# Optimization experiments

Hardware: AMD Instinct MI355X
Metric: run time of the kernel (lower is better)

## Reference

```python
import jax, jax.numpy as jnp
import numpy as np

B, SC, ST = 16, 512, 512
DP, DC = 256, 128
D = DP + 2 * DC          # 512 = d_model
H, L, DFF = 8, 2, 2048
NCAT, NCONT = 1000, 2048


def sin_embed(vals, d, scale=1000.0):
    # vectorized sinusoidal_time_embedding: even dims -> sin(angle), odd dims -> cos(angle)
    i = jnp.arange(d, dtype=jnp.float32)
    ang = vals.astype(jnp.float32)[..., None] / jnp.power(scale, i / d)
    return jnp.where(i % 2 == 0, jnp.sin(ang), jnp.cos(ang))


def layer_norm(x, g, b, eps=1e-5):
    m = jnp.mean(x, -1, keepdims=True)
    v = jnp.mean(jnp.square(x - m), -1, keepdims=True)
    return (x - m) / jnp.sqrt(v + eps) * g + b


def setup_inputs() -> dict:
    key = jax.random.key(0)
    ks = jax.random.split(key, 16)
    s = 0.02
    def n(k, shape, scale=s):
        return jax.random.normal(k, shape, dtype=jnp.float32) * scale
    return {
        "context_cat": jax.random.randint(ks[0], (B, SC), 0, NCAT),
        "context_time": jax.random.uniform(ks[1], (B, SC), dtype=jnp.float32) * 100.0,
        "context_f0": jax.random.uniform(ks[2], (B, SC), dtype=jnp.float32) * 500.0,
        "target_cat": jax.random.randint(ks[3], (B, ST), 0, NCAT),
        "target_time": jax.random.uniform(ks[4], (B, ST), dtype=jnp.float32) * 100.0,
        "target_f0": jax.random.uniform(ks[5], (B, ST), dtype=jnp.float32) * 500.0,
        "cat_table": n(ks[6], (NCAT, DP), 1.0),
        "cont_table": sin_embed(jnp.arange(NCONT, dtype=jnp.float32), DC),  # frozen sin table
        "pad_emb": n(ks[7], (D,), 1.0),
        "Wq": n(ks[8], (L, D, D)), "bq": jnp.zeros((L, D)),
        "Wk": n(ks[9], (L, D, D)), "bk": jnp.zeros((L, D)),
        "Wv": n(ks[10], (L, D, D)), "bv": jnp.zeros((L, D)),
        "Wo": n(ks[11], (L, D, D)), "bo": jnp.zeros((L, D)),
        "ln1g": jnp.ones((L, D)), "ln1b": jnp.zeros((L, D)),
        "ln2g": jnp.ones((L, D)), "ln2b": jnp.zeros((L, D)),
        "W1": n(ks[12], (L, D, DFF)), "b1": jnp.zeros((L, DFF)),
        "W2": n(ks[13], (L, DFF, D)), "b2": jnp.zeros((L, D)),
    }


def reference(context_cat, context_time, context_f0, target_cat, target_time, target_f0,
              cat_table, cont_table, pad_emb,
              Wq, bq, Wk, bk, Wv, bv, Wo, bo,
              ln1g, ln1b, ln2g, ln2b, W1, b1, W2, b2):
    def embed(cat, tm, f0):
        pad = cat < 0
        e = jnp.concatenate(
            [cat_table[jnp.maximum(cat, 0)], sin_embed(tm, DC), sin_embed(f0, DC)], axis=-1)
        return jnp.where(pad[..., None], pad_emb, e), pad

    ce, cp = embed(context_cat, context_time, context_f0)
    te, tp = embed(target_cat, target_time, target_f0)
    x = jnp.concatenate([ce, te], axis=1)                       # [B, SC+ST, D]
    bias = jnp.where(jnp.concatenate([cp, tp], 1), -1e9, 0.0)[:, None, None, :]
    hd = D // H
    inv_sqrt = 1.0 / np.sqrt(hd).astype(np.float32)

    def step(h, p):
        wq, bq_, wk, bk_, wv, bv_, wo, bo_, g1, c1, g2, c2, w1, d1, w2, d2 = p
        Bn, S, _ = h.shape
        q = (h @ wq + bq_).reshape(Bn, S, H, hd)
        k = (h @ wk + bk_).reshape(Bn, S, H, hd)
        v = (h @ wv + bv_).reshape(Bn, S, H, hd)
        scores = jnp.einsum('bqhd,bkhd->bhqk', q, k) * inv_sqrt + bias
        attn = jax.nn.softmax(scores, axis=-1)
        o = jnp.einsum('bhqk,bkhd->bqhd', attn, v).reshape(Bn, S, D)
        h = layer_norm(h + o @ wo + bo_, g1, c1)                # post-norm (torch default)
        f = jax.nn.relu(h @ w1 + d1) @ w2 + d2
        return layer_norm(h + f, g2, c2), None

    x, _ = jax.lax.scan(step, x, (Wq, bq, Wk, bk, Wv, bv, Wo, bo,
                                  ln1g, ln1b, ln2g, ln2b, W1, b1, W2, b2))
    out = x[:, SC:, :]
    pred_cat = out[..., :DP] @ cat_table.T
    pred_time = out[..., DP:DP + DC] @ cont_table.T
    pred_f0 = out[..., DP + DC:] @ cont_table.T
    return pred_cat, pred_time, pred_f0
```

## Files before the change

### kernel.cpp

```cpp
#include <hip/hip_runtime.h>


typedef _Float16 half8 __attribute__((ext_vector_type(8)));
typedef _Float16 half4 __attribute__((ext_vector_type(4)));
typedef float f32x4 __attribute__((ext_vector_type(4)));
typedef unsigned int uint2v __attribute__((ext_vector_type(2)));
typedef unsigned int uint4v __attribute__((ext_vector_type(4)));

__device__ __forceinline__ void gl2lds16(const _Float16* g, _Float16* l) {
    __builtin_amdgcn_global_load_lds(
        (const __attribute__((address_space(1))) void*)g,
        (__attribute__((address_space(3))) void*)l, 16, 0, 0);
}

__global__ void cast_f32_f16_k(const float* __restrict__ in, _Float16* __restrict__ out,
                               long nsrc, long ntot) {
    long i = (long)blockIdx.x * blockDim.x + threadIdx.x;
    long stride = (long)gridDim.x * blockDim.x;
    for (; i < ntot; i += stride) out[i] = i < nsrc ? (_Float16)in[i] : (_Float16)0.f;
}

__global__ void tcast_k(const float* __restrict__ in, _Float16* __restrict__ out,
                        int R, int C, long zs, int rowoff) {
    __shared__ float tile[32][33];
    long z = blockIdx.z;
    const float* src = in + z * (long)R * C;
    _Float16* dst = out + z * zs + (long)rowoff * R;
    int c0 = blockIdx.x * 32, r0 = blockIdx.y * 32;
    for (int i = threadIdx.y; i < 32; i += 8)
        tile[i][threadIdx.x] = src[(long)(r0 + i) * C + c0 + threadIdx.x];
    __syncthreads();
    for (int i = threadIdx.y; i < 32; i += 8)
        dst[(long)(c0 + i) * R + r0 + threadIdx.x] = (_Float16)tile[threadIdx.x][i];
}

__global__ void bcat_k(const float* __restrict__ bq, const float* __restrict__ bk,
                       const float* __restrict__ bv, float* __restrict__ out, int L) {
    int i = blockIdx.x * 256 + threadIdx.x;
    if (i >= L * 1536) return;
    int l = i / 1536, j = i - l * 1536;
    float v = j < 512 ? bq[l * 512 + j] : (j < 1024 ? bk[l * 512 + j - 512] : bv[l * 512 + j - 1024]);
    out[i] = v;
}

__global__ void vtrans_k(const _Float16* __restrict__ qkv, _Float16* __restrict__ vT) {
    __shared__ _Float16 tile[32][33];
    int bh = blockIdx.z; int b = bh >> 3, h = bh & 7;
    int s0 = blockIdx.x * 32, d0 = blockIdx.y * 32;
    const _Float16* src = qkv + ((long)b * 1024) * 1536 + 1024 + h * 64;
    _Float16* dst = vT + (long)bh * 64 * 1024;
    for (int i = threadIdx.y; i < 32; i += 8)
        tile[i][threadIdx.x] = src[(long)(s0 + i) * 1536 + d0 + threadIdx.x];
    __syncthreads();
    for (int i = threadIdx.y; i < 32; i += 8)
        dst[(long)(d0 + i) * 1024 + s0 + threadIdx.x] = tile[threadIdx.x][i];
}

__global__ __launch_bounds__(128) void embed_k(
    const int* __restrict__ ccat, const float* __restrict__ ctime, const float* __restrict__ cf0,
    const int* __restrict__ tcat, const float* __restrict__ ttime, const float* __restrict__ tf0,
    const float* __restrict__ cat_table, const float* __restrict__ pad_emb,
    _Float16* __restrict__ xb, float* __restrict__ biasKey) {
    int t = blockIdx.x;
    int b = t >> 10, s = t & 1023;
    int j = b * 512 + (s & 511);
    int cat; float tm, f0;
    if (s < 512) { cat = ccat[j]; tm = ctime[j]; f0 = cf0[j]; }
    else         { cat = tcat[j]; tm = ttime[j]; f0 = tf0[j]; }
    bool pad = cat < 0;
    if (threadIdx.x == 0) biasKey[t] = pad ? -1e9f : 0.f;
    int c = cat < 0 ? 0 : cat;
    half4 h4;
    #pragma unroll
    for (int u = 0; u < 4; u++) {
        int d = threadIdx.x * 4 + u;
        float val;
        if (pad) val = pad_emb[d];
        else if (d < 256) val = cat_table[(long)c * 256 + d];
        else {
            float base = (d < 384) ? tm : f0;
            int i = (d < 384) ? (d - 256) : (d - 384);
            float ang = base / powf(1000.f, (float)i * (1.f / 128.f));
            val = (i & 1) ? cosf(ang) : sinf(ang);
        }
        h4[u] = (_Float16)val;
    }
    *(half4*)&xb[(long)t * 512 + threadIdx.x * 4] = h4;
}

__global__ __launch_bounds__(256) void layernorm_k(
    const _Float16* __restrict__ in, _Float16* __restrict__ out,
    const float* __restrict__ g, const float* __restrict__ beta) {
    long row = blockIdx.x;
    int tid = threadIdx.x;
    const unsigned* rw = (const unsigned*)(in + row * 512);
    unsigned wo = rw[tid];
    float v0 = (float)(_Float16)__builtin_bit_cast(_Float16, (unsigned short)(wo & 0xffff));
    float v1 = (float)(_Float16)__builtin_bit_cast(_Float16, (unsigned short)(wo >> 16));
    float s = v0 + v1, q = v0 * v0 + v1 * v1;
    #pragma unroll
    for (int o = 32; o; o >>= 1) { s += __shfl_down(s, o); q += __shfl_down(q, o); }
    __shared__ float rs[4], rq[4];
    if ((tid & 63) == 0) { rs[tid >> 6] = s; rq[tid >> 6] = q; }
    __syncthreads();
    s = rs[0] + rs[1] + rs[2] + rs[3];
    q = rq[0] + rq[1] + rq[2] + rq[3];
    float mean = s * (1.f / 512.f);
    float var = q * (1.f / 512.f) - mean * mean;
    float rstd = rsqrtf(var + 1e-5f);
    float y0 = (v0 - mean) * rstd * g[tid * 2] + beta[tid * 2];
    float y1 = (v1 - mean) * rstd * g[tid * 2 + 1] + beta[tid * 2 + 1];
    unsigned short u0 = __builtin_bit_cast(unsigned short, (_Float16)y0);
    unsigned short u1 = __builtin_bit_cast(unsigned short, (_Float16)y1);
    ((unsigned*)(out + row * 512))[tid] = (unsigned)u0 | ((unsigned)u1 << 16);
}

__global__ __launch_bounds__(512, 4) void flash_k(
    const _Float16* __restrict__ QKV, const _Float16* __restrict__ VT,
    const float* __restrict__ biasKey, _Float16* __restrict__ O) {
    const int S = 1024, D = 512, LDQ = 1536, NT = 16;
    int bh = blockIdx.x; int b = bh >> 3, h = bh & 7;
    int qt = blockIdx.y;
    int tid = threadIdx.x, w = tid >> 6, lane = tid & 63;
    int g = lane >> 4, q15 = lane & 15;

    __shared__ __align__(16) _Float16 Ks[2][64 * 64];
    __shared__ __align__(16) _Float16 VTs[2][64 * 64];
    __shared__ __align__(16) float biasLds[1024];

    {
        const float* bsrc = biasKey + (long)b * S;
        biasLds[tid]       = bsrc[tid] * 1.442695041f;
        biasLds[tid + 512] = bsrc[tid + 512] * 1.442695041f;
    }

    int qrow = qt * 128 + w * 16 + q15;
    const _Float16* qp = QKV + ((long)(b * S + qrow)) * LDQ + h * 64 + g * 8;
    half8 qf[2];
    qf[0] = *(const half8*)(qp);
    qf[1] = *(const half8*)(qp + 32);
    const _Float16 qsc = (_Float16)0.1803368801f;
    #pragma unroll
    for (int kk = 0; kk < 2; kk++)
        #pragma unroll
        for (int i = 0; i < 8; i++) qf[kk][i] *= qsc;

    const _Float16* kbase = QKV + 512 + ((long)b * S) * LDQ + h * 64;
    const _Float16* vbase = VT + (long)bh * 64 * S;

    auto stageK = [&](int buf, int kt) {
        int row = tid >> 3, p = tid & 7;
        int s = p ^ (row & 7);
        gl2lds16(kbase + (long)(kt * 64 + row) * LDQ + s * 8, &Ks[buf][tid * 8]);
    };
    auto stageV = [&](int buf, int kt) {
        int row = tid >> 3, p = tid & 7;
        int s = p ^ (row & 7);
        gl2lds16(vbase + (long)row * S + kt * 64 + s * 8, &VTs[buf][tid * 8]);
    };

    f32x4 acc_o[4];
    #pragma unroll
    for (int i = 0; i < 4; i++)
        #pragma unroll
        for (int r = 0; r < 4; r++) acc_o[i][r] = 0.f;
    float m_run = -1e30f, l_run = 0.f;
    bool gOdd = (g & 1) != 0;

    auto QK = [&](int kt, f32x4 (&s)[4]) {
        #pragma unroll
        for (int mf = 0; mf < 4; mf++)
            s[mf] = *(const f32x4*)&biasLds[kt * 64 + mf * 16 + g * 4];
        int buf = kt & 1;
        __builtin_amdgcn_s_setprio(1);
        #pragma unroll
        for (int kk = 0; kk < 2; kk++)
            #pragma unroll
            for (int mf = 0; mf < 4; mf++) {
                int row = mf * 16 + q15;
                half8 kf = *(const half8*)&Ks[buf][row * 64 + (((kk * 4 + g) ^ (row & 7)) * 8)];
                s[mf] = __builtin_amdgcn_mfma_f32_16x16x32_f16(kf, qf[kk], s[mf], 0, 0, 0);
            }
        __builtin_amdgcn_s_setprio(0);
    };

    auto SMPV = [&](int kt, f32x4 (&s)[4]) {
        float t0 = fmaxf(fmaxf(s[0][0], s[0][1]), fmaxf(s[0][2], s[0][3]));
        float t1 = fmaxf(fmaxf(s[1][0], s[1][1]), fmaxf(s[1][2], s[1][3]));
        float t2 = fmaxf(fmaxf(s[2][0], s[2][1]), fmaxf(s[2][2], s[2][3]));
        float t3 = fmaxf(fmaxf(s[3][0], s[3][1]), fmaxf(s[3][2], s[3][3]));
        float mt = fmaxf(fmaxf(t0, t1), fmaxf(t2, t3));
        mt = fmaxf(mt, __shfl_xor(mt, 16));
        mt = fmaxf(mt, __shfl_xor(mt, 32));

        float rsum = 0.f;
        if (__all(mt - m_run <= 8.f)) {
            #pragma unroll
            for (int mf = 0; mf < 4; mf++)
                #pragma unroll
                for (int r = 0; r < 4; r++) {
                    float p = exp2f(s[mf][r] - m_run);
                    s[mf][r] = p; rsum += p;
                }
        } else {
            float m_new = fmaxf(m_run, mt);
            float scale = exp2f(m_run - m_new);
            #pragma unroll
            for (int mf = 0; mf < 4; mf++)
                #pragma unroll
                for (int r = 0; r < 4; r++) {
                    float p = exp2f(s[mf][r] - m_new);
                    s[mf][r] = p; rsum += p;
                }
            float sc[4];
            #pragma unroll
            for (int r = 0; r < 4; r++) sc[r] = __shfl(scale, g * 4 + r);
            #pragma unroll
            for (int nf = 0; nf < 4; nf++)
                #pragma unroll
                for (int r = 0; r < 4; r++) acc_o[nf][r] *= sc[r];
            l_run *= scale;
            m_run = m_new;
        }
        rsum += __shfl_xor(rsum, 16);
        rsum += __shfl_xor(rsum, 32);
        l_run += rsum;

        unsigned pk[4][2];
        #pragma unroll
        for (int mf = 0; mf < 4; mf++) {
            auto h0 = __builtin_amdgcn_cvt_pkrtz(s[mf][0], s[mf][1]);
            auto h1 = __builtin_amdgcn_cvt_pkrtz(s[mf][2], s[mf][3]);
            pk[mf][0] = __builtin_bit_cast(unsigned, h0);
            pk[mf][1] = __builtin_bit_cast(unsigned, h1);
        }

        int buf = kt & 1;
        #pragma unroll
        for (int kk = 0; kk < 2; kk++) {
            unsigned wA[2], wB[2];
            #pragma unroll
            for (int wi = 0; wi < 2; wi++) {
                uint2v r2 = __builtin_amdgcn_permlane32_swap(
                    pk[2 * kk][wi], pk[2 * kk + 1][wi], false, false);
                unsigned na = r2[0];
                unsigned nb = r2[1];
                unsigned sa = (unsigned)__builtin_amdgcn_ds_swizzle((int)na, 0x401F);
                unsigned sb = (unsigned)__builtin_amdgcn_ds_swizzle((int)nb, 0x401F);
                wA[wi] = gOdd ? sb : na;
                wB[wi] = gOdd ? nb : sa;
            }
            uint4v paw;
            paw[0] = wA[0]; paw[1] = wA[1]; paw[2] = wB[0]; paw[3] = wB[1];
            half8 pa = __builtin_bit_cast(half8, paw);
            __builtin_amdgcn_s_setprio(1);
            #pragma unroll
            for (int nf = 0; nf < 4; nf++) {
                int row = nf * 16 + q15;
                half8 vf = *(const half8*)&VTs[buf][row * 64 + (((kk * 4 + g) ^ (row & 7)) * 8)];
                acc_o[nf] = __builtin_amdgcn_mfma_f32_16x16x32_f16(pa, vf, acc_o[nf], 0, 0, 0);
            }
            __builtin_amdgcn_s_setprio(0);
        }
    };

    f32x4 sA[4], sB[4];
    stageK(0, 0); stageV(0, 0); stageK(1, 1);
    __syncthreads();
    QK(0, sA);

    for (int t = 0; t < NT; t += 2) {
        __syncthreads();
        if (t + 2 < NT) stageK(t & 1, t + 2);
        if (t + 1 < NT) stageV((t + 1) & 1, t + 1);
        if (t + 1 < NT) QK(t + 1, sB);
        SMPV(t, sA);
        __syncthreads();
        if (t + 3 < NT) stageK((t + 1) & 1, t + 3);
        if (t + 2 < NT) stageV(t & 1, t + 2);
        if (t + 2 < NT) QK(t + 2, sA);
        SMPV(t + 1, sB);
    }

    float linv = 1.f / l_run;
    float lv[4];
    #pragma unroll
    for (int r = 0; r < 4; r++) lv[r] = __shfl(linv, g * 4 + r);
    _Float16* obase = O + ((long)(b * S + qt * 128 + w * 16)) * D + h * 64;
    #pragma unroll
    for (int nf = 0; nf < 4; nf++)
        #pragma unroll
        for (int r = 0; r < 4; r++) {
            int row = g * 4 + r;
            obase[(long)row * D + nf * 16 + q15] = (_Float16)(acc_o[nf][r] * lv[r]);
        }
}

template<int NBUF>
__global__ __launch_bounds__(256) void gemm_nt(
    const _Float16* __restrict__ A, long lda, long sA1, long sA2,
    const _Float16* __restrict__ Bm, long ldb, long sB1, long sB2,
    float* Cf, _Float16* Cb, long ldc, long sC1, long sC2,
    const float* __restrict__ bias, long sb1, long sb2,
    const _Float16* resid,
    int M, int N, int K, int Z2, float alpha, int relu) {
    int z = blockIdx.z;
    int z1 = z / Z2, z2 = z - z1 * Z2;
    A  += z1 * sA1 + z2 * sA2;
    Bm += z1 * sB1 + z2 * sB2;
    long coff = z1 * sC1 + z2 * sC2;
    if (bias) bias += z1 * sb1 + z2 * sb2;

    int gx = gridDim.x;
    int nwg = gx * gridDim.y;
    int bid = blockIdx.y * gx + blockIdx.x;
    int q = nwg >> 3, r = nwg & 7;
    int xcd = bid & 7, ii = bid >> 3;
    int swz = (xcd < r ? xcd * (q + 1) : r * (q + 1) + (xcd - r) * q) + ii;
    int m0 = (swz / gx) * 128;
    int n0 = (swz % gx) * 128;

    __shared__ __align__(16) _Float16 As[NBUF][128 * 32];
    __shared__ __align__(16) _Float16 Bs[NBUF][128 * 32];

    int tid = threadIdx.x;
    int lane = tid & 63;
    int w = tid >> 6;
    int wr = (w >> 1) << 6;
    int wc = (w & 1) << 6;

    f32x4 acc[4][4];
    #pragma unroll
    for (int i = 0; i < 4; i++)
        #pragma unroll
        for (int jj = 0; jj < 4; jj++) { acc[i][jj][0] = 0.f; acc[i][jj][1] = 0.f; acc[i][jj][2] = 0.f; acc[i][jj][3] = 0.f; }

    int fr = lane & 15;
    int g = lane >> 4;
    int rs8 = (g ^ (fr & 3)) * 8;

    auto stage = [&](int buf, int kt) {
        #pragma unroll
        for (int i = 0; i < 2; i++) {
            int idx = tid + i * 256;
            int row = idx >> 2, s = idx & 3;
            int sg = s ^ (row & 3);
            gl2lds16(A + (long)(m0 + row) * lda + kt * 32 + sg * 8, &As[buf][idx * 8]);
            gl2lds16(Bm + (long)(n0 + row) * ldb + kt * 32 + sg * 8, &Bs[buf][idx * 8]);
        }
    };

    auto compute = [&](int cur) {
        half8 af[4], bfv[4];
        #pragma unroll
        for (int m = 0; m < 4; m++) af[m] = *(const half8*)&As[cur][(wr + m * 16 + fr) * 32 + rs8];
        #pragma unroll
        for (int n = 0; n < 4; n++) bfv[n] = *(const half8*)&Bs[cur][(wc + n * 16 + fr) * 32 + rs8];
        #pragma unroll
        for (int m = 0; m < 4; m++)
            #pragma unroll
            for (int n = 0; n < 4; n++)
                acc[m][n] = __builtin_amdgcn_mfma_f32_16x16x32_f16(af[m], bfv[n], acc[m][n], 0, 0, 0);
    };

    int nk = K >> 5;
    if constexpr (NBUF == 2) {
        stage(0, 0);
        for (int t = 0; t < nk; ++t) {
            __builtin_amdgcn_s_barrier();
            if (t + 1 < nk) {
                stage((t + 1) & 1, t + 1);
                asm volatile("s_waitcnt vmcnt(4)" ::: "memory");
            } else {
                asm volatile("s_waitcnt vmcnt(0)" ::: "memory");
            }
            __builtin_amdgcn_s_barrier();
            __builtin_amdgcn_sched_barrier(0);
            compute(t & 1);
        }
    } else {
        stage(0, 0);
        if (nk > 1) stage(1, 1);
        if (nk > 2) stage(2, 2);
        for (int t = 0; t < nk; ++t) {
            if (t + 2 < nk)      asm volatile("s_waitcnt vmcnt(8)" ::: "memory");
            else if (t + 1 < nk) asm volatile("s_waitcnt vmcnt(4)" ::: "memory");
            else                 asm volatile("s_waitcnt vmcnt(0)" ::: "memory");
            __builtin_amdgcn_s_barrier();
            __builtin_amdgcn_sched_barrier(0);
            if (t + 3 < nk) stage((t + 3) & 3, t + 3);
            compute(t & 3);
        }
    }

    int fq = lane >> 4;
    #pragma unroll
    for (int m = 0; m < 4; m++) {
        #pragma unroll
        for (int jj = 0; jj < 4; jj++) {
            long row = m0 + wr + m * 16 + fq * 4 + jj;
            #pragma unroll
            for (int n = 0; n < 4; n++) {
                int col = n0 + wc + n * 16 + fr;
                if (col < N) {
                    float v = acc[m][n][jj] * alpha;
                    if (bias) v += bias[col];
                    long o = coff + row * ldc + col;
                    if (resid) v += (float)resid[o];
                    if (relu) v = fmaxf(v, 0.f);
                    if (Cf) Cf[o] = v;
                    if (Cb) Cb[o] = (_Float16)v;
                }
            }
        }
    }
}

extern "C" void kernel_launch(void* const* d_in, const int* in_sizes, int n_in,
                              void* d_out, int out_size, void* d_ws, size_t ws_size,
                              hipStream_t stream) {
    const int Bn = 16, S = 1024, D = 512, H = 8, L = 2, DFF = 2048, NCAT = 1000, NCONT = 2048;
    const long M = (long)Bn * S;

    const int*   ccat      = (const int*)d_in[0];
    const float* ctime     = (const float*)d_in[1];
    const float* cf0       = (const float*)d_in[2];
    const int*   tcat      = (const int*)d_in[3];
    const float* ttime     = (const float*)d_in[4];
    const float* tf0       = (const float*)d_in[5];
    const float* cat_table = (const float*)d_in[6];
    const float* cont_tab  = (const float*)d_in[7];
    const float* pad_emb   = (const float*)d_in[8];
    const float* Wq = (const float*)d_in[9];
    const float* bq = (const float*)d_in[10];
    const float* Wk = (const float*)d_in[11];
    const float* bk = (const float*)d_in[12];
    const float* Wv = (const float*)d_in[13];
    const float* bv = (const float*)d_in[14];
    const float* Wo = (const float*)d_in[15];
    const float* bo = (const float*)d_in[16];
    const float* ln1g = (const float*)d_in[17];
    const float* ln1b = (const float*)d_in[18];
    const float* ln2g = (const float*)d_in[19];
    const float* ln2b = (const float*)d_in[20];
    const float* W1 = (const float*)d_in[21];
    const float* b1 = (const float*)d_in[22];
    const float* W2 = (const float*)d_in[23];
    const float* b2 = (const float*)d_in[24];

    char* wsb = (char*)d_ws;
    size_t off = 0;
    auto alloc = [&](size_t bytes) -> void* {
        off = (off + 255) & ~(size_t)255;
        void* p = wsb + off; off += bytes; return p;
    };

    _Float16*  xb      = (_Float16*)alloc(M * D * 2);
    _Float16*  tb      = (_Float16*)alloc(M * D * 2);
    _Float16*  hb      = (_Float16*)alloc(M * D * 2);
    _Float16*  qkv     = (_Float16*)alloc(M * 3 * D * 2);
    _Float16*  vT      = (_Float16*)alloc(M * D * 2);
    _Float16*  ob      = (_Float16*)alloc(M * D * 2);
    float*     biasKey = (float*)alloc(M * 4);
    _Float16*  WqkvT = (_Float16*)alloc((size_t)L * 3 * D * D * 2);
    float*     bqkv  = (float*)alloc((size_t)L * 3 * D * 4);
    _Float16*  WoT  = (_Float16*)alloc((size_t)L * D * D * 2);
    _Float16*  W1T  = (_Float16*)alloc((size_t)L * D * DFF * 2);
    _Float16*  W2T  = (_Float16*)alloc((size_t)L * DFF * D * 2);
    _Float16*  catT = (_Float16*)alloc((size_t)1024 * 256 * 2);
    _Float16*  conT = (_Float16*)alloc((size_t)NCONT * 128 * 2);

    size_t need_ffh = (size_t)M * DFF * 2;
    _Float16* ffh;
    size_t offAl = (off + 255) & ~(size_t)255;
    if (offAl + need_ffh <= ws_size) ffh = (_Float16*)alloc(need_ffh);
    else ffh = (_Float16*)d_out;

    auto gemm = [&](const _Float16* A, long lda, long sA1, long sA2,
                    const _Float16* Bm, long ldb, long sB1, long sB2,
                    float* Cf, _Float16* Cb, long ldc, long sC1, long sC2,
                    const float* bias, long sb1, long sb2,
                    const _Float16* resid, int Mm, int Nn, int Kk,
                    int Z1, int Z2, float alpha, int relu, int deep) {
        dim3 gdim((Nn + 127) / 128, (Mm + 127) / 128, Z1 * Z2);
        if (deep)
            gemm_nt<4><<<gdim, 256, 0, stream>>>(A, lda, sA1, sA2, Bm, ldb, sB1, sB2,
                                                 Cf, Cb, ldc, sC1, sC2, bias, sb1, sb2,
                                                 resid, Mm, Nn, Kk, Z2, alpha, relu);
        else
            gemm_nt<2><<<gdim, 256, 0, stream>>>(A, lda, sA1, sA2, Bm, ldb, sB1, sB2,
                                                 Cf, Cb, ldc, sC1, sC2, bias, sb1, sb2,
                                                 resid, Mm, Nn, Kk, Z2, alpha, relu);
    };

    dim3 tb8(32, 8);
    tcast_k<<<dim3(D / 32, D / 32, L), tb8, 0, stream>>>(Wq, WqkvT, D, D, (long)3 * D * D, 0);
    tcast_k<<<dim3(D / 32, D / 32, L), tb8, 0, stream>>>(Wk, WqkvT, D, D, (long)3 * D * D, D);
    tcast_k<<<dim3(D / 32, D / 32, L), tb8, 0, stream>>>(Wv, WqkvT, D, D, (long)3 * D * D, 2 * D);
    bcat_k<<<dim3((L * 1536 + 255) / 256), 256, 0, stream>>>(bq, bk, bv, bqkv, L);
    tcast_k<<<dim3(D / 32, D / 32, L), tb8, 0, stream>>>(Wo, WoT, D, D, (long)D * D, 0);
    tcast_k<<<dim3(DFF / 32, D / 32, L), tb8, 0, stream>>>(W1, W1T, D, DFF, (long)D * DFF, 0);
    tcast_k<<<dim3(D / 32, DFF / 32, L), tb8, 0, stream>>>(W2, W2T, DFF, D, (long)DFF * D, 0);
    cast_f32_f16_k<<<dim3(512), 256, 0, stream>>>(cat_table, catT, (long)NCAT * 256, (long)1024 * 256);
    cast_f32_f16_k<<<dim3(512), 256, 0, stream>>>(cont_tab, conT, (long)NCONT * 128, (long)NCONT * 128);

    embed_k<<<dim3((unsigned)M), 128, 0, stream>>>(ccat, ctime, cf0, tcat, ttime, tf0,
                                                   cat_table, pad_emb, xb, biasKey);

    for (int l = 0; l < L; l++) {
        gemm(xb, D, 0, 0, WqkvT + (size_t)l * 3 * D * D, D, 0, 0, nullptr, qkv, 3 * D, 0, 0,
             bqkv + (size_t)l * 3 * D, 0, 0, nullptr, (int)M, 3 * D, D, 1, 1, 1.f, 0, 0);
        vtrans_k<<<dim3(32, 2, Bn * H), tb8, 0, stream>>>(qkv, vT);

        flash_k<<<dim3(Bn * H, S / 128), 512, 0, stream>>>(qkv, vT, biasKey, ob);

        gemm(ob, D, 0, 0, WoT + (size_t)l * D * D, D, 0, 0, nullptr, tb, D, 0, 0,
             bo + l * D, 0, 0, xb, (int)M, D, D, 1, 1, 1.f, 0, 1);
        layernorm_k<<<dim3((unsigned)M), 256, 0, stream>>>(tb, hb, ln1g + l * D, ln1b + l * D);

        gemm(hb, D, 0, 0, W1T + (size_t)l * D * DFF, D, 0, 0, nullptr, ffh, DFF, 0, 0,
             b1 + l * DFF, 0, 0, nullptr, (int)M, DFF, D, 1, 1, 1.f, 1, 0);
        gemm(ffh, DFF, 0, 0, W2T + (size_t)l * DFF * D, DFF, 0, 0, nullptr, tb, D, 0, 0,
             b2 + l * D, 0, 0, hb, (int)M, D, DFF, 1, 1, 1.f, 0, 1);
        layernorm_k<<<dim3((unsigned)M), 256, 0, stream>>>(tb, xb, ln2g + l * D, ln2b + l * D);
    }

    float* out_cat  = (float*)d_out;
    float* out_time = out_cat + (size_t)Bn * 512 * NCAT;
    float* out_f0   = out_time + (size_t)Bn * 512 * NCONT;
    gemm(xb + (size_t)512 * D, D, (long)S * D, 0,
         catT, 256, 0, 0,
         out_cat, nullptr, NCAT, (long)512 * NCAT, 0,
         nullptr, 0, 0, nullptr, 512, NCAT, 256, Bn, 1, 1.f, 0, 0);
    gemm(xb + (size_t)512 * D + 256, D, (long)S * D, 128,
         conT, 128, 0, 0,
         out_time, nullptr, NCONT, (long)512 * NCONT, (long)Bn * 512 * NCONT,
         nullptr, 0, 0, nullptr, 512, NCONT, 128, Bn, 2, 1.f, 0, 0);
}
```

Before: 842.8 us.

## Fuse V transpose into QKV GEMM epilogue and use BK=64 double-buffered deep GEMM

Result: no change. 856.5 us (+1.6%).

```diff
diff --git a/kernel.cpp b/kernel.cpp
--- a/kernel.cpp
+++ b/kernel.cpp
@@ -41,19 +41,6 @@
     int l = i / 1536, j = i - l * 1536;
     float v = j < 512 ? bq[l * 512 + j] : (j < 1024 ? bk[l * 512 + j - 512] : bv[l * 512 + j - 1024]);
     out[i] = v;
-}
-
-__global__ void vtrans_k(const _Float16* __restrict__ qkv, _Float16* __restrict__ vT) {
-    __shared__ _Float16 tile[32][33];
-    int bh = blockIdx.z; int b = bh >> 3, h = bh & 7;
-    int s0 = blockIdx.x * 32, d0 = blockIdx.y * 32;
-    const _Float16* src = qkv + ((long)b * 1024) * 1536 + 1024 + h * 64;
-    _Float16* dst = vT + (long)bh * 64 * 1024;
-    for (int i = threadIdx.y; i < 32; i += 8)
-        tile[i][threadIdx.x] = src[(long)(s0 + i) * 1536 + d0 + threadIdx.x];
-    __syncthreads();
-    for (int i = threadIdx.y; i < 32; i += 8)
-        dst[(long)(d0 + i) * 1024 + s0 + threadIdx.x] = tile[threadIdx.x][i];
 }
 
 __global__ __launch_bounds__(128) void embed_k(
@@ -296,14 +283,18 @@
         }
 }
 
-template<int NBUF>
+template<int MODE>
 __global__ __launch_bounds__(256) void gemm_nt(
     const _Float16* __restrict__ A, long lda, long sA1, long sA2,
     const _Float16* __restrict__ Bm, long ldb, long sB1, long sB2,
     float* Cf, _Float16* Cb, long ldc, long sC1, long sC2,
     const float* __restrict__ bias, long sb1, long sb2,
-    const _Float16* resid,
+    const _Float16* resid, _Float16* vt,
     int M, int N, int K, int Z2, float alpha, int relu) {
+    constexpr int BK = MODE ? 64 : 32;
+    constexpr int SLOTS = BK / 8;
+    constexpr int LPS = (128 * BK / 8) / 256;
+
     int z = blockIdx.z;
     int z1 = z / Z2, z2 = z - z1 * Z2;
     A  += z1 * sA1 + z2 * sA2;
@@ -320,8 +311,8 @@
     int m0 = (swz / gx) * 128;
     int n0 = (swz % gx) * 128;
 
-    __shared__ __align__(16) _Float16 As[NBUF][128 * 32];
-    __shared__ __align__(16) _Float16 Bs[NBUF][128 * 32];
+    __shared__ __align__(16) _Float16 As[2][128 * BK];
+    __shared__ __align__(16) _Float16 Bs[2][128 * BK];
 
     int tid = threadIdx.x;
     int lane = tid & 63;
@@ -337,60 +328,56 @@
 
     int fr = lane & 15;
     int g = lane >> 4;
-    int rs8 = (g ^ (fr & 3)) * 8;
 
     auto stage = [&](int buf, int kt) {
         #pragma unroll
-        for (int i = 0; i < 2; i++) {
+        for (int i = 0; i < LPS; i++) {
             int idx = tid + i * 256;
-            int row = idx >> 2, s = idx & 3;
-            int sg = s ^ (row & 3);
-            gl2lds16(A + (long)(m0 + row) * lda + kt * 32 + sg * 8, &As[buf][idx * 8]);
-            gl2lds16(Bm + (long)(n0 + row) * ldb + kt * 32 + sg * 8, &Bs[buf][idx * 8]);
+            int row = idx / SLOTS, s = idx % SLOTS;
+            int sg = s ^ (row & (SLOTS - 1));
+            gl2lds16(A + (long)(m0 + row) * lda + kt * BK + sg * 8, &As[buf][idx * 8]);
+            gl2lds16(Bm + (long)(n0 + row) * ldb + kt * BK + sg * 8, &Bs[buf][idx * 8]);
         }
     };
 
     auto compute = [&](int cur) {
-        half8 af[4], bfv[4];
-        #pragma unroll
-        for (int m = 0; m < 4; m++) af[m] = *(const half8*)&As[cur][(wr + m * 16 + fr) * 32 + rs8];
-        #pragma unroll
-        for (int n = 0; n < 4; n++) bfv[n] = *(const half8*)&Bs[cur][(wc + n * 16 + fr) * 32 + rs8];
-        #pragma unroll
-        for (int m = 0; m < 4; m++)
-            #pragma unroll
-            for (int n = 0; n < 4; n++)
-                acc[m][n] = __builtin_amdgcn_mfma_f32_16x16x32_f16(af[m], bfv[n], acc[m][n], 0, 0, 0);
-    };
-
-    int nk = K >> 5;
-    if constexpr (NBUF == 2) {
-        stage(0, 0);
-        for (int t = 0; t < nk; ++t) {
-            __builtin_amdgcn_s_barrier();
-            if (t + 1 < nk) {
-                stage((t + 1) & 1, t + 1);
+        #pragma unroll
+        for (int kk = 0; kk < BK / 32; kk++) {
+            half8 af[4], bfv[4];
+            #pragma unroll
+            for (int m = 0; m < 4; m++) {
+                int row = wr + m * 16 + fr;
+                af[m] = *(const half8*)&As[cur][row * BK + (((kk * 4 + g) ^ (row & (SLOTS - 1))) * 8)];
+            }
+            #pragma unroll
+            for (int n = 0; n < 4; n++) {
+                int row = wc + n * 16 + fr;
+                bfv[n] = *(const half8*)&Bs[cur][row * BK + (((kk * 4 + g) ^ (row & (SLOTS - 1))) * 8)];
+            }
+            #pragma unroll
+            for (int m = 0; m < 4; m++)
+                #pragma unroll
+                for (int n = 0; n < 4; n++)
+                    acc[m][n] = __builtin_amdgcn_mfma_f32_16x16x32_f16(af[m], bfv[n], acc[m][n], 0, 0, 0);
+        }
+    };
+
+    int nk = K / BK;
+    stage(0, 0);
+    for (int t = 0; t < nk; ++t) {
+        __builtin_amdgcn_s_barrier();
+        if (t + 1 < nk) {
+            stage((t + 1) & 1, t + 1);
+            if constexpr (MODE == 0)
                 asm volatile("s_waitcnt vmcnt(4)" ::: "memory");
-            } else {
-                asm volatile("s_waitcnt vmcnt(0)" ::: "memory");
-            }
-            __builtin_amdgcn_s_barrier();
-            __builtin_amdgcn_sched_barrier(0);
-            compute(t & 1);
-        }
-    } else {
-        stage(0, 0);
-        if (nk > 1) stage(1, 1);
-        if (nk > 2) stage(2, 2);
-        for (int t = 0; t < nk; ++t) {
-            if (t + 2 < nk)      asm volatile("s_waitcnt vmcnt(8)" ::: "memory");
-            else if (t + 1 < nk) asm volatile("s_waitcnt vmcnt(4)" ::: "memory");
-            else                 asm volatile("s_waitcnt vmcnt(0)" ::: "memory");
-            __builtin_amdgcn_s_barrier();
-            __builtin_amdgcn_sched_barrier(0);
-            if (t + 3 < nk) stage((t + 3) & 3, t + 3);
-            compute(t & 3);
-        }
+            else
+                asm volatile("s_waitcnt vmcnt(8)" ::: "memory");
+        } else {
+            asm volatile("s_waitcnt vmcnt(0)" ::: "memory");
+        }
+        __builtin_amdgcn_s_barrier();
+        __builtin_amdgcn_sched_barrier(0);
+        compute(t & 1);
     }
 
     int fq = lane >> 4;
@@ -405,11 +392,17 @@
                 if (col < N) {
                     float v = acc[m][n][jj] * alpha;
                     if (bias) v += bias[col];
-                    long o = coff + row * ldc + col;
-                    if (resid) v += (float)resid[o];
-                    if (relu) v = fmaxf(v, 0.f);
-                    if (Cf) Cf[o] = v;
-                    if (Cb) Cb[o] = (_Float16)v;
+                    if (vt && col >= 1024) {
+                        int dv = col - 1024;
+                        long bh = (row >> 10) * 8 + (dv >> 6);
+                        vt[bh * 65536 + (long)(dv & 63) * 1024 + (row & 1023)] = (_Float16)v;
+                    } else {
+                        long o = coff + row * ldc + col;
+                        if (resid) v += (float)resid[o];
+                        if (relu) v = fmaxf(v, 0.f);
+                        if (Cf) Cf[o] = v;
+                        if (Cb) Cb[o] = (_Float16)v;
+                    }
                 }
             }
         }
@@ -480,17 +473,17 @@
                     const _Float16* Bm, long ldb, long sB1, long sB2,
                     float* Cf, _Float16* Cb, long ldc, long sC1, long sC2,
                     const float* bias, long sb1, long sb2,
-                    const _Float16* resid, int Mm, int Nn, int Kk,
+                    const _Float16* resid, _Float16* vt, int Mm, int Nn, int Kk,
                     int Z1, int Z2, float alpha, int relu, int deep) {
         dim3 gdim((Nn + 127) / 128, (Mm + 127) / 128, Z1 * Z2);
         if (deep)
-            gemm_nt<4><<<gdim, 256, 0, stream>>>(A, lda, sA1, sA2, Bm, ldb, sB1, sB2,
+            gemm_nt<1><<<gdim, 256, 0, stream>>>(A, lda, sA1, sA2, Bm, ldb, sB1, sB2,
                                                  Cf, Cb, ldc, sC1, sC2, bias, sb1, sb2,
-                                                 resid, Mm, Nn, Kk, Z2, alpha, relu);
+                                                 resid, vt, Mm, Nn, Kk, Z2, alpha, relu);
         else
-            gemm_nt<2><<<gdim, 256, 0, stream>>>(A, lda, sA1, sA2, Bm, ldb, sB1, sB2,
+            gemm_nt<0><<<gdim, 256, 0, stream>>>(A, lda, sA1, sA2, Bm, ldb, sB1, sB2,
                                                  Cf, Cb, ldc, sC1, sC2, bias, sb1, sb2,
-                                                 resid, Mm, Nn, Kk, Z2, alpha, relu);
+                                                 resid, vt, Mm, Nn, Kk, Z2, alpha, relu);
     };
 
     dim3 tb8(32, 8);
@@ -509,19 +502,18 @@
 
     for (int l = 0; l < L; l++) {
         gemm(xb, D, 0, 0, WqkvT + (size_t)l * 3 * D * D, D, 0, 0, nullptr, qkv, 3 * D, 0, 0,
-             bqkv + (size_t)l * 3 * D, 0, 0, nullptr, (int)M, 3 * D, D, 1, 1, 1.f, 0, 0);
-        vtrans_k<<<dim3(32, 2, Bn * H), tb8, 0, stream>>>(qkv, vT);
+             bqkv + (size_t)l * 3 * D, 0, 0, nullptr, vT, (int)M, 3 * D, D, 1, 1, 1.f, 0, 0);
 
         flash_k<<<dim3(Bn * H, S / 128), 512, 0, stream>>>(qkv, vT, biasKey, ob);
 
         gemm(ob, D, 0, 0, WoT + (size_t)l * D * D, D, 0, 0, nullptr, tb, D, 0, 0,
-             bo + l * D, 0, 0, xb, (int)M, D, D, 1, 1, 1.f, 0, 1);
+             bo + l * D, 0, 0, xb, nullptr, (int)M, D, D, 1, 1, 1.f, 0, 1);
         layernorm_k<<<dim3((unsigned)M), 256, 0, stream>>>(tb, hb, ln1g + l * D, ln1b + l * D);
 
         gemm(hb, D, 0, 0, W1T + (size_t)l * D * DFF, D, 0, 0, nullptr, ffh, DFF, 0, 0,
-             b1 + l * DFF, 0, 0, nullptr, (int)M, DFF, D, 1, 1, 1.f, 1, 0);
+             b1 + l * DFF, 0, 0, nullptr, nullptr, (int)M, DFF, D, 1, 1, 1.f, 1, 0);
         gemm(ffh, DFF, 0, 0, W2T + (size_t)l * DFF * D, DFF, 0, 0, nullptr, tb, D, 0, 0,
-             b2 + l * D, 0, 0, hb, (int)M, D, DFF, 1, 1, 1.f, 0, 1);
+             b2 + l * D, 0, 0, hb, nullptr, (int)M, D, DFF, 1, 1, 1.f, 0, 1);
         layernorm_k<<<dim3((unsigned)M), 256, 0, stream>>>(tb, xb, ln2g + l * D, ln2b + l * D);
     }
 
@@ -531,9 +523,9 @@
     gemm(xb + (size_t)512 * D, D, (long)S * D, 0,
          catT, 256, 0, 0,
          out_cat, nullptr, NCAT, (long)512 * NCAT, 0,
-         nullptr, 0, 0, nullptr, 512, NCAT, 256, Bn, 1, 1.f, 0, 0);
+         nullptr, 0, 0, nullptr, nullptr, 512, NCAT, 256, Bn, 1, 1.f, 0, 0);
     gemm(xb + (size_t)512 * D + 256, D, (long)S * D, 128,
          conT, 128, 0, 0,
          out_time, nullptr, NCONT, (long)512 * NCONT, (long)Bn * 512 * NCONT,
-         nullptr, 0, 0, nullptr, 512, NCONT, 128, Bn, 2, 1.f, 0, 0);
-}
+         nullptr, 0, 0, nullptr, nullptr, 512, NCONT, 128, Bn, 2, 1.f, 0, 0);
+}
```
